# Optimization experiments

Hardware: AMD Instinct MI355X
Metric: run time of the kernel (lower is better)

## Reference

```python
import jax, jax.numpy as jnp
import numpy as np
import math

H = 16          # num_heads
MAX_REL = 512   # max_relative_positions


def setup_inputs() -> dict:
    key = jax.random.key(0)
    ks = jax.random.split(key, 8)
    B, N, Hd = 1, 2048, 1024
    s = 0.05  # keep activations numerically tame
    return {
        "hidden_states": jax.random.normal(ks[0], (B, N, Hd), jnp.float32),
        "attention_mask": jnp.ones((B, N, N), jnp.int32),
        "W_in": jax.random.normal(ks[1], (3 * Hd, Hd), jnp.float32) * s,
        "q_bias": jax.random.normal(ks[2], (Hd,), jnp.float32) * s,
        "v_bias": jax.random.normal(ks[3], (Hd,), jnp.float32) * s,
        "W_pos": jax.random.normal(ks[4], (Hd, Hd), jnp.float32) * s,
        "W_posq": jax.random.normal(ks[5], (Hd, Hd), jnp.float32) * s,
        "b_posq": jax.random.normal(ks[6], (Hd,), jnp.float32) * s,
        "rel_emb": jax.random.normal(ks[7], (2 * MAX_REL, Hd), jnp.float32) * s,
    }


def reference(hidden_states, attention_mask, W_in, q_bias, v_bias, W_pos, W_posq, b_posq, rel_emb):
    B, N, Hd = hidden_states.shape
    d = Hd // H
    span = min(N, MAX_REL)
    scale_factor = 3  # 1 + c2p + p2c

    # in_proj then DeBERTa-style head split: [B,N,H,3d] -> chunk last dim
    qp = jnp.einsum('bnk,ok->bno', hidden_states, W_in).reshape(B, N, H, 3 * d)
    q, k, v = jnp.split(qp, 3, axis=-1)            # each [B,N,H,d]
    q = q.transpose(0, 2, 1, 3)                    # [B,H,N,d]
    k = k.transpose(0, 2, 1, 3)
    v = v.transpose(0, 2, 1, 3)
    q = q + q_bias.reshape(H, d)[None, :, None, :]
    v = v + v_bias.reshape(H, d)[None, :, None, :]

    q = q / math.sqrt(d * scale_factor)
    scores = jnp.einsum('bhid,bhjd->bhij', q, k)   # content-to-content

    # relative position table, sliced around center
    rel = rel_emb[MAX_REL - span: MAX_REL + span]                     # [2span,Hd]
    pos_k = jnp.einsum('sk,ok->so', rel, W_pos).reshape(2 * span, H, d).transpose(1, 0, 2)   # [H,2span,d]
    pos_q = (jnp.einsum('sk,ok->so', rel, W_posq) + b_posq).reshape(2 * span, H, d).transpose(1, 0, 2)
    pos_q = pos_q / math.sqrt(d * scale_factor)

    rp = jnp.arange(N)[:, None] - jnp.arange(N)[None, :]              # [N,N] rel pos q->k
    c2p_idx = jnp.clip(rp + span, 0, 2 * span - 1)                    # [N,N]
    p2c_idx = jnp.clip(-rp + span, 0, 2 * span - 1)

    # content-to-position: gather along span axis
    c2p = jnp.einsum('bhid,hsd->bhis', q, pos_k)                      # [B,H,N,2span]
    c2p = jnp.take_along_axis(c2p, c2p_idx[None, None], axis=-1)      # [B,H,N,N]

    # position-to-content: gather then transpose(-1,-2)
    p2c = jnp.einsum('bhjd,hsd->bhjs', k, pos_q)                      # [B,H,N,2span]
    p2c = jnp.take_along_axis(p2c, p2c_idx[None, None], axis=-1)      # [B,H,j,i]
    p2c = p2c.transpose(0, 1, 3, 2)                                   # [B,H,i,j]

    scores = scores + c2p + p2c

    # XSoftmax: mask-fill with dtype min, softmax, re-zero masked
    mask = attention_mask.astype(bool)[:, None]                       # [B,1,N,N]
    neg = jnp.finfo(scores.dtype).min
    probs = jax.nn.softmax(jnp.where(mask, scores, neg), axis=-1)
    probs = jnp.where(mask, probs, 0.0)

    ctx = jnp.einsum('bhij,bhjd->bhid', probs, v)                     # [B,H,N,d]
    return ctx.transpose(0, 2, 1, 3).reshape(B, N, Hd)
```

## Files before the change

kernel.cpp:

```cpp
#include <hip/hip_runtime.h>

#define SEQ   2048
#define HID   1024
#define NHEAD 16
#define DH    64
#define S2    1024

typedef short bf16x8 __attribute__((ext_vector_type(8)));
typedef float f32x4  __attribute__((ext_vector_type(4)));

static __device__ __forceinline__ short f2bf(float f) {
    unsigned u = __float_as_uint(f);
    unsigned r = (u + 0x7fffu + ((u >> 16) & 1u)) >> 16;
    return (short)r;
}
static __device__ __forceinline__ float bf2f(short h) {
    return __uint_as_float(((unsigned)(unsigned short)h) << 16);
}
static __device__ __forceinline__ int wbase(int a) {
    int b = a < 0 ? 0 : (a > 952 ? 952 : a);
    return b & ~7;
}


__global__ __launch_bounds__(256) void cvt_bf16_k(const float* __restrict__ in,
                                                  short* __restrict__ out, int n8) {
    int idx = blockIdx.x * 256 + threadIdx.x;
    if (idx < n8) {
        const float4 a = ((const float4*)in)[idx * 2];
        const float4 b = ((const float4*)in)[idx * 2 + 1];
        bf16x8 r;
        r[0] = f2bf(a.x); r[1] = f2bf(a.y); r[2] = f2bf(a.z); r[3] = f2bf(a.w);
        r[4] = f2bf(b.x); r[5] = f2bf(b.y); r[6] = f2bf(b.z); r[7] = f2bf(b.w);
        ((bf16x8*)out)[idx] = r;
    }
}

__global__ __launch_bounds__(256) void cvt3_bf16_k(
    const float* __restrict__ in0, const float* __restrict__ in1, const float* __restrict__ in2,
    short* __restrict__ out0, short* __restrict__ out1, short* __restrict__ out2) {
    int b = blockIdx.x, sel = b >> 9;
    int idx = (b & 511) * 256 + threadIdx.x;
    const float* in = sel == 0 ? in0 : (sel == 1 ? in1 : in2);
    short* out = sel == 0 ? out0 : (sel == 1 ? out1 : out2);
    const float4 a = ((const float4*)in)[idx * 2];
    const float4 b4 = ((const float4*)in)[idx * 2 + 1];
    bf16x8 r;
    r[0] = f2bf(a.x); r[1] = f2bf(a.y); r[2] = f2bf(a.z); r[3] = f2bf(a.w);
    r[4] = f2bf(b4.x); r[5] = f2bf(b4.y); r[6] = f2bf(b4.z); r[7] = f2bf(b4.w);
    ((bf16x8*)out)[idx] = r;
}

__global__ __launch_bounds__(256) void maskflag_k(const int* __restrict__ amask, int* __restrict__ flags)
{
    __shared__ int sall[4], sany[4];
    const int jt = blockIdx.x, it = blockIdx.y;
    const int tid = threadIdx.x;
    const int r = tid >> 2, cseg = (tid & 3) << 4;
    const int4* rp = (const int4*)(amask + (size_t)(it * 64 + r) * SEQ + jt * 64 + cseg);
    int allnz = 1, anynz = 0;
    #pragma unroll
    for (int e = 0; e < 4; ++e) {
        int4 v = rp[e];
        allnz &= (v.x != 0) & (v.y != 0) & (v.z != 0) & (v.w != 0);
        anynz |= (v.x != 0) | (v.y != 0) | (v.z != 0) | (v.w != 0);
    }
    unsigned long long ba = __ballot(allnz != 0);
    unsigned long long bo = __ballot(anynz != 0);
    const int w = tid >> 6;
    if ((tid & 63) == 0) { sall[w] = (ba == ~0ull); sany[w] = (bo != 0ull); }
    __syncthreads();
    if (tid == 0) {
        int all4 = sall[0] & sall[1] & sall[2] & sall[3];
        int any4 = sany[0] | sany[1] | sany[2] | sany[3];
        flags[it * 32 + jt] = all4 ? 2 : (any4 ? 1 : 0);
    }
}

static __device__ __forceinline__ void gemm_tile(
    const short* __restrict__ Ag, int lda,
    const short* __restrict__ Bg, int ldb,
    int K, short* As, short* Bs, f32x4 (&acc)[4][2])
{
    const int tid = threadIdx.x;
    const int lane = tid & 63, w = tid >> 6;
    const int g = lane >> 4, ln = lane & 15;
    const int wm = (w >> 1) * 64, wn = (w & 1) * 32;
    for (int kt = 0; kt < K; kt += 64) {
        __syncthreads();
        #pragma unroll
        for (int it = 0; it < 4; ++it) {
            int c = it * 256 + tid;
            int r = c >> 3, cb = c & 7;
            uint4 v = *(const uint4*)(Ag + (size_t)r * lda + kt + ((cb ^ (r & 7)) << 3));
            *(uint4*)(As + r * 64 + cb * 8) = v;
        }
        #pragma unroll
        for (int it = 0; it < 2; ++it) {
            int c = it * 256 + tid;
            int r = c >> 3, cb = c & 7;
            uint4 v = *(const uint4*)(Bg + (size_t)r * ldb + kt + ((cb ^ (r & 7)) << 3));
            *(uint4*)(Bs + r * 64 + cb * 8) = v;
        }
        __syncthreads();
        #pragma unroll
        for (int k0 = 0; k0 < 2; ++k0) {
            bf16x8 bfr[2];
            #pragma unroll
            for (int nf = 0; nf < 2; ++nf) {
                int rr = wn + nf * 16 + ln;
                int kc = (k0 * 4 + g) ^ (rr & 7);
                bfr[nf] = *(const bf16x8*)(Bs + rr * 64 + kc * 8);
            }
            #pragma unroll
            for (int mf = 0; mf < 4; ++mf) {
                int rr = wm + mf * 16 + ln;
                int kc = (k0 * 4 + g) ^ (rr & 7);
                bf16x8 afr = *(const bf16x8*)(As + rr * 64 + kc * 8);
                #pragma unroll
                for (int nf = 0; nf < 2; ++nf)
                    acc[mf][nf] = __builtin_amdgcn_mfma_f32_16x16x32_bf16(afr, bfr[nf], acc[mf][nf], 0, 0, 0);
            }
        }
    }
}

__global__ __launch_bounds__(256) void qkv_mfma_k(
    const short* __restrict__ hid, const short* __restrict__ win,
    const float* __restrict__ q_bias, const float* __restrict__ v_bias,
    short* __restrict__ qT, short* __restrict__ kT, short* __restrict__ vTt)
{
    __shared__ __align__(16) short As[128 * 64];
    __shared__ __align__(16) short Bs[64 * 64];
    const int tid = threadIdx.x, lane = tid & 63, w = tid >> 6;
    const int g = lane >> 4, ln = lane & 15;
    const int wm = (w >> 1) * 64, wn = (w & 1) * 32;
    const int m0 = blockIdx.y * 128, n0 = blockIdx.x * 64;
    f32x4 acc[4][2] = {};
    gemm_tile(hid + (size_t)m0 * HID, HID, win + (size_t)n0 * HID, HID, HID, As, Bs, acc);
    const float inv_s = 0.07216878364870323f * 1.4426950408889634f;
    #pragma unroll
    for (int nf = 0; nf < 2; ++nf) {
        const int n = n0 + wn + nf * 16 + ln;
        const int h = n / 192, c = n % 192;
        #pragma unroll
        for (int mf = 0; mf < 4; ++mf) {
            const int mb = m0 + wm + mf * 16 + 4 * g;
            if (c < 64) {
                float qb = q_bias[h * 64 + c];
                #pragma unroll
                for (int reg = 0; reg < 4; ++reg)
                    qT[((size_t)h * SEQ + mb + reg) * DH + c] = f2bf((acc[mf][nf][reg] + qb) * inv_s);
            } else if (c < 128) {
                #pragma unroll
                for (int reg = 0; reg < 4; ++reg)
                    kT[((size_t)h * SEQ + mb + reg) * DH + (c - 64)] = f2bf(acc[mf][nf][reg]);
            } else {
                float vb = v_bias[h * 64 + (c - 128)];
                short4 s4;
                s4.x = f2bf(acc[mf][nf][0] + vb);
                s4.y = f2bf(acc[mf][nf][1] + vb);
                s4.z = f2bf(acc[mf][nf][2] + vb);
                s4.w = f2bf(acc[mf][nf][3] + vb);
                *(short4*)(vTt + ((size_t)h * DH + (c - 128)) * SEQ + mb) = s4;
            }
        }
    }
}

__global__ __launch_bounds__(256) void pos_mfma_k(
    const short* __restrict__ rel, const short* __restrict__ wpos, const short* __restrict__ wposq,
    const float* __restrict__ b_posq, short* __restrict__ posk, short* __restrict__ posq)
{
    __shared__ __align__(16) short As[128 * 64];
    __shared__ __align__(16) short Bs[64 * 64];
    const int tid = threadIdx.x, lane = tid & 63, w = tid >> 6;
    const int g = lane >> 4, ln = lane & 15;
    const int wm = (w >> 1) * 64, wn = (w & 1) * 32;
    const int m0 = blockIdx.y * 128, n0 = blockIdx.x * 64;
    const int which = blockIdx.z;
    const short* Bg = (which ? wposq : wpos) + (size_t)n0 * HID;
    f32x4 acc[4][2] = {};
    gemm_tile(rel + (size_t)m0 * HID, HID, Bg, HID, HID, As, Bs, acc);
    const float inv_s = 0.07216878364870323f * 1.4426950408889634f;
    #pragma unroll
    for (int mf = 0; mf < 4; ++mf) {
        #pragma unroll
        for (int nf = 0; nf < 2; ++nf) {
            #pragma unroll
            for (int reg = 0; reg < 4; ++reg) {
                int s = m0 + wm + mf * 16 + 4 * g + reg;
                int o = n0 + wn + nf * 16 + ln;
                int h = o >> 6, c = o & 63;
                float v = acc[mf][nf][reg];
                if (which) posq[((size_t)h * S2 + s) * DH + c] = f2bf((v + b_posq[o]) * inv_s);
                else       posk[((size_t)h * S2 + s) * DH + c] = f2bf(v);
            }
        }
    }
}

__global__ __launch_bounds__(256) void band_mfma_k(
    const short* __restrict__ qT, const short* __restrict__ kT,
    const short* __restrict__ posk, const short* __restrict__ posq,
    short* __restrict__ c2p, short* __restrict__ p2c)
{
    __shared__ __align__(16) short Xs[128 * 64];
    __shared__ __align__(16) short Ps[64 * 64];
    const int tid = threadIdx.x, lane = tid & 63, w = tid >> 6;
    const int g = lane >> 4, ln = lane & 15;
    const int m0 = blockIdx.y * 128, n0 = blockIdx.x * 64;
    const int head = blockIdx.z >> 1, which = blockIdx.z & 1;
    const short* Xg = (which ? kT : qT) + (size_t)head * SEQ * DH + (size_t)m0 * DH;
    const short* Pg = (which ? posq : posk) + (size_t)head * S2 * DH + (size_t)n0 * DH;
    short* outb = (which ? p2c : c2p) + (size_t)head * SEQ * S2;
    #pragma unroll
    for (int it = 0; it < 4; ++it) {
        int c = it * 256 + tid;
        int r = c >> 3, cb = c & 7;
        *(uint4*)(Xs + r * 64 + cb * 8) = *(const uint4*)(Xg + (size_t)r * DH + ((cb ^ (r & 7)) << 3));
    }
    #pragma unroll
    for (int it = 0; it < 2; ++it) {
        int c = it * 256 + tid;
        int r = c >> 3, cb = c & 7;
        *(uint4*)(Ps + r * 64 + cb * 8) = *(const uint4*)(Pg + (size_t)r * DH + ((cb ^ (r & 7)) << 3));
    }
    __syncthreads();
    const int wm = w * 32;
    f32x4 acc[2][4] = {};
    #pragma unroll
    for (int k0 = 0; k0 < 2; ++k0) {
        bf16x8 af[4];
        #pragma unroll
        for (int nf = 0; nf < 4; ++nf) {
            int rr = nf * 16 + ln;
            af[nf] = *(const bf16x8*)(Ps + rr * 64 + (((k0 * 4 + g) ^ (rr & 7)) << 3));
        }
        #pragma unroll
        for (int mf = 0; mf < 2; ++mf) {
            int rr = wm + mf * 16 + ln;
            bf16x8 xf = *(const bf16x8*)(Xs + rr * 64 + (((k0 * 4 + g) ^ (rr & 7)) << 3));
            #pragma unroll
            for (int nf = 0; nf < 4; ++nf)
                acc[mf][nf] = __builtin_amdgcn_mfma_f32_16x16x32_bf16(af[nf], xf, acc[mf][nf], 0, 0, 0);
        }
    }
    #pragma unroll
    for (int mf = 0; mf < 2; ++mf) {
        const int m = m0 + wm + mf * 16 + ln;
        #pragma unroll
        for (int nf = 0; nf < 4; ++nf) {
            short4 s4;
            s4.x = f2bf(acc[mf][nf][0]);
            s4.y = f2bf(acc[mf][nf][1]);
            s4.z = f2bf(acc[mf][nf][2]);
            s4.w = f2bf(acc[mf][nf][3]);
            *(short4*)(outb + (size_t)m * S2 + n0 + nf * 16 + 4 * g) = s4;
        }
    }
}

__global__ __launch_bounds__(256) void attn_mfma_k(
    const short* __restrict__ qT, const short* __restrict__ kT, const short* __restrict__ vTt,
    const short* __restrict__ c2p, const short* __restrict__ p2c,
    const int* __restrict__ amask, const int* __restrict__ flags,
    float* __restrict__ out)
{
    __shared__ __align__(16) char pool[69632];
    short* const lds = (short*)pool;
    const int tid = threadIdx.x, lane = tid & 63, w = tid >> 6;
    const int g = lane >> 4, ln = lane & 15;
    const int h = blockIdx.y, it = blockIdx.x;
    const int i0 = it * 64;
    const int iw = i0 + w * 16;
    const short* qh = qT + (size_t)h * SEQ * DH;
    const short* kh = kT + (size_t)h * SEQ * DH;
    const short* vh = vTt + (size_t)h * DH * SEQ;
    const short* ch = c2p + (size_t)h * SEQ * S2;
    const short* ph = p2c + (size_t)h * SEQ * S2;

    bf16x8 aq[2];
    aq[0] = *(const bf16x8*)(qh + (size_t)(iw + ln) * DH + 0  + g * 8);
    aq[1] = *(const bf16x8*)(qh + (size_t)(iw + ln) * DH + 32 + g * 8);

    f32x4 o4[4] = {};
    float mrow = -1.0e30f, lrow = 0.f;

    const int fbase = it * 32;
    const int r0 = tid >> 3,          cb0 = tid & 7;
    const int r1 = (256 + tid) >> 3,  cb1 = tid & 7;
    const int ksw0 = (cb0 ^ (r0 & 7)) << 3, ksw1 = (cb1 ^ (r1 & 7)) << 3;
    const int wr = tid >> 2, wu = (tid & 3) * 16;

    uint4 kr0, kr1, vr0, vr1, cw0, cw1, pw0, pw1, cw2, pw2;

    auto issue = [&](int jt) {
        const int j0 = jt * 64;
        kr0 = *(const uint4*)(kh + (size_t)(j0 + r0) * DH + ksw0);
        vr0 = *(const uint4*)(vh + (size_t)r0 * SEQ + j0 + ksw0);
        kr1 = *(const uint4*)(kh + (size_t)(j0 + r1) * DH + ksw1);
        vr1 = *(const uint4*)(vh + (size_t)r1 * SEQ + j0 + ksw1);
        int bc = wbase(i0 + wr - j0 + 449);
        cw0 = *(const uint4*)(ch + (size_t)(i0 + wr) * S2 + bc + wu);
        cw1 = *(const uint4*)(ch + (size_t)(i0 + wr) * S2 + bc + wu + 8);
        int bp = wbase(i0 - j0 - wr + 512);
        pw0 = *(const uint4*)(ph + (size_t)(j0 + wr) * S2 + bp + wu);
        pw1 = *(const uint4*)(ph + (size_t)(j0 + wr) * S2 + bp + wu + 8);
        if (tid < 64) {
            int bc2 = wbase(i0 + tid - j0 + 449);
            cw2 = *(const uint4*)(ch + (size_t)(i0 + tid) * S2 + bc2 + 64);
            int bp2 = wbase(i0 - j0 - tid + 512);
            pw2 = *(const uint4*)(ph + (size_t)(j0 + tid) * S2 + bp2 + 64);
        }
    };
    auto commit = [&](int bo) {
        short* Ks  = lds + bo;
        short* Vs  = lds + bo + 4096;
        short* Phw = lds + bo + 8192;
        short* Chw = lds + bo + 12800;
        *(uint4*)(Ks + r0 * 64 + cb0 * 8) = kr0;
        *(uint4*)(Vs + r0 * 64 + cb0 * 8) = vr0;
        *(uint4*)(Ks + r1 * 64 + cb1 * 8) = kr1;
        *(uint4*)(Vs + r1 * 64 + cb1 * 8) = vr1;
        *(uint4*)(Chw + wr * 72 + wu) = cw0;
        *(uint4*)(Chw + wr * 72 + wu + 8) = cw1;
        *(uint4*)(Phw + wr * 72 + wu) = pw0;
        *(uint4*)(Phw + wr * 72 + wu + 8) = pw1;
        if (tid < 64) {
            *(uint4*)(Chw + tid * 72 + 64) = cw2;
            *(uint4*)(Phw + tid * 72 + 64) = pw2;
        }
    };

    issue(0);
    int flag_cur = flags[fbase];
    commit(0);
    __syncthreads();

    const int il = w * 16 + ln;
    const int i  = i0 + il;

    int bo = 0;
    for (int t = 0; t < 32; ++t) {
        const int j0 = t * 64;
        int flag_next = 0;
        if (t < 31) { flag_next = flags[fbase + t + 1]; issue(t + 1); }

        short* Ks  = lds + bo;
        short* Vs  = lds + bo + 4096;
        short* Phw = lds + bo + 8192;
        short* Chw = lds + bo + 12800;
        short* Psw = Chw + w * 1152;

        if (flag_cur != 0) {
            f32x4 sfr[4];
            #pragma unroll
            for (int nf = 0; nf < 4; ++nf) sfr[nf] = (f32x4){0.f, 0.f, 0.f, 0.f};
            __builtin_amdgcn_s_setprio(1);
            #pragma unroll
            for (int k0 = 0; k0 < 2; ++k0) {
                #pragma unroll
                for (int nf = 0; nf < 4; ++nf) {
                    int rr = nf * 16 + ln;
                    bf16x8 ak = *(const bf16x8*)(Ks + rr * 64 + (((k0 * 4 + g) ^ (rr & 7)) << 3));
                    sfr[nf] = __builtin_amdgcn_mfma_f32_16x16x32_bf16(ak, aq[k0], sfr[nf], 0, 0, 0);
                }
            }
            __builtin_amdgcn_s_setprio(0);

            const int d = i0 - j0;
            float p[4][4];
            if (d >= -448 && d <= 384 && flag_cur == 2) {
                const int a = i - j0 + 449;
                const short* Cb = Chw + il * 72 + (a & 7) - 4 * g;
                const int cg = d + 512 - 4 * g;
                const int pbase = il + 288 * g;
                const int pb0 = pbase + (cg & 7);
                const int pb1 = pbase + ((cg - 1) & 7);
                const int pb2 = pbase + ((cg - 2) & 7);
                const int pb3 = pbase + ((cg - 3) & 7);
                #pragma unroll
                for (int nf = 0; nf < 4; ++nf) {
                    p[nf][0] = sfr[nf][0] + bf2f(Cb[63 - 16 * nf - 0]) + bf2f(Phw[pb0 + 1152 * nf + 0]);
                    p[nf][1] = sfr[nf][1] + bf2f(Cb[63 - 16 * nf - 1]) + bf2f(Phw[pb1 + 1152 * nf + 72]);
                    p[nf][2] = sfr[nf][2] + bf2f(Cb[63 - 16 * nf - 2]) + bf2f(Phw[pb2 + 1152 * nf + 144]);
                    p[nf][3] = sfr[nf][3] + bf2f(Cb[63 - 16 * nf - 3]) + bf2f(Phw[pb3 + 1152 * nf + 216]);
                }
            } else if (flag_cur == 2 && (d <= -576 || d >= 576)) {
                const int q = d < 0 ? 0 : 71;
                const float cb = bf2f(Chw[il * 72 + q]);
                #pragma unroll
                for (int nf = 0; nf < 4; ++nf) {
                    const int pb = (16 * nf + 4 * g) * 72 + q;
                    p[nf][0] = sfr[nf][0] + cb + bf2f(Phw[pb]);
                    p[nf][1] = sfr[nf][1] + cb + bf2f(Phw[pb + 72]);
                    p[nf][2] = sfr[nf][2] + cb + bf2f(Phw[pb + 144]);
                    p[nf][3] = sfr[nf][3] + cb + bf2f(Phw[pb + 216]);
                }
            } else {
                const short* Crow = Chw + il * 72 - wbase(i - j0 + 449);
                const int Cc = i0 - j0 + 512;
                #pragma unroll
                for (int nf = 0; nf < 4; ++nf) {
                    #pragma unroll
                    for (int reg = 0; reg < 4; ++reg) {
                        int jr = 16 * nf + 4 * g + reg;
                        int s = i - (j0 + jr) + 512; s = s < 0 ? 0 : (s > 1023 ? 1023 : s);
                        int wbp = Cc - jr; wbp = wbp < 0 ? 0 : (wbp > 952 ? 952 : wbp); wbp &= ~7;
                        float sc = sfr[nf][reg] + bf2f(Crow[s]) + bf2f(Phw[jr * 72 + (s - wbp)]);
                        if (flag_cur != 2)
                            sc = amask[(size_t)i * SEQ + (j0 + jr)] ? sc : -1.0e30f;
                        p[nf][reg] = sc;
                    }
                }
            }

            float mx = p[0][0];
            #pragma unroll
            for (int nf = 0; nf < 4; ++nf)
                #pragma unroll
                for (int reg = 0; reg < 4; ++reg) mx = fmaxf(mx, p[nf][reg]);
            mx = fmaxf(mx, __shfl_xor(mx, 16, 64));
            mx = fmaxf(mx, __shfl_xor(mx, 32, 64));
            float nm = fmaxf(mrow, mx);
            float sc, rs = 0.f;
            if (flag_cur == 2) {
                sc = exp2f(mrow - nm);
                #pragma unroll
                for (int nf = 0; nf < 4; ++nf)
                    #pragma unroll
                    for (int reg = 0; reg < 4; ++reg) {
                        float e = exp2f(p[nf][reg] - nm);
                        p[nf][reg] = e; rs += e;
                    }
            } else {
                bool live = nm > -5.0e29f;
                sc = live ? exp2f(mrow - nm) : 1.f;
                #pragma unroll
                for (int nf = 0; nf < 4; ++nf)
                    #pragma unroll
                    for (int reg = 0; reg < 4; ++reg) {
                        float e = live ? exp2f(p[nf][reg] - nm) : 0.f;
                        p[nf][reg] = e; rs += e;
                    }
            }
            rs += __shfl_xor(rs, 16, 64);
            rs += __shfl_xor(rs, 32, 64);
            lrow = lrow * sc + rs;
            mrow = nm;

            #pragma unroll
            for (int nf = 0; nf < 4; ++nf) {
                short4 s4;
                s4.x = f2bf(p[nf][0]); s4.y = f2bf(p[nf][1]);
                s4.z = f2bf(p[nf][2]); s4.w = f2bf(p[nf][3]);
                *(short4*)(Psw + ln * 72 + 16 * nf + 4 * g) = s4;
            }

            #pragma unroll
            for (int mf = 0; mf < 4; ++mf)
                #pragma unroll
                for (int reg = 0; reg < 4; ++reg) o4[mf][reg] *= sc;

            __builtin_amdgcn_s_setprio(1);
            #pragma unroll
            for (int k0 = 0; k0 < 2; ++k0) {
                bf16x8 bp = *(const bf16x8*)(Psw + ln * 72 + k0 * 32 + g * 8);
                #pragma unroll
                for (int mf = 0; mf < 4; ++mf) {
                    int rr = mf * 16 + ln;
                    bf16x8 av = *(const bf16x8*)(Vs + rr * 64 + (((k0 * 4 + g) ^ (rr & 7)) << 3));
                    o4[mf] = __builtin_amdgcn_mfma_f32_16x16x32_bf16(av, bp, o4[mf], 0, 0, 0);
                }
            }
            __builtin_amdgcn_s_setprio(0);
        }

        if (t < 31) commit(bo ^ 17408);
        __syncthreads();
        bo ^= 17408;
        flag_cur = flag_next;
    }

    float rinv = (mrow > -5.0e29f && lrow > 0.f) ? 1.f / lrow : 0.f;
    __syncthreads();
    float* Tf = (float*)pool;
    #pragma unroll
    for (int mf = 0; mf < 4; ++mf)
        #pragma unroll
        for (int reg = 0; reg < 4; ++reg)
            Tf[(w * 16 + ln) * 68 + mf * 16 + 4 * g + reg] = o4[mf][reg] * rinv;
    __syncthreads();
    {
        const int r = tid >> 2, sgm = (tid & 3) << 4;
        float* dst = out + (size_t)(i0 + r) * HID + h * 64 + sgm;
        #pragma unroll
        for (int k = 0; k < 4; ++k)
            ((float4*)dst)[k] = *(float4*)(Tf + r * 68 + sgm + k * 4);
    }
}

extern "C" void kernel_launch(void* const* d_in, const int* in_sizes, int n_in,
                              void* d_out, int out_size, void* d_ws, size_t ws_size,
                              hipStream_t stream)
{
    const float* hidden  = (const float*)d_in[0];
    const int*   amask   = (const int*)  d_in[1];
    const float* W_in    = (const float*)d_in[2];
    const float* q_bias  = (const float*)d_in[3];
    const float* v_bias  = (const float*)d_in[4];
    const float* W_pos   = (const float*)d_in[5];
    const float* W_posq  = (const float*)d_in[6];
    const float* b_posq  = (const float*)d_in[7];
    const float* rel_emb = (const float*)d_in[8];
    float* out = (float*)d_out;

    short* ws = (short*)d_ws;
    short* qT   = ws;
    short* kT   = ws + 2097152;
    short* vTt  = ws + 4194304;
    short* c2p  = ws + 6291456;
    short* p2c  = ws + 39845888;
    short* scr      = ws + 73400320;
    short* hid_bf   = scr;
    short* win_bf   = scr + 2097152;
    short* rel_bf   = scr;
    short* wpos_bf  = scr + 1048576;
    short* wposq_bf = scr + 2097152;
    short* posk     = scr + 3145728;
    short* posq     = scr + 4194304;
    int*   flags    = (int*)(scr + 8650752);

    cvt_bf16_k<<<1024, 256, 0, stream>>>(hidden, hid_bf, 262144);
    cvt_bf16_k<<<1536, 256, 0, stream>>>(W_in, win_bf, 393216);
    maskflag_k<<<dim3(32, 32), 256, 0, stream>>>(amask, flags);
    qkv_mfma_k<<<dim3(48, 16), 256, 0, stream>>>(hid_bf, win_bf, q_bias, v_bias, qT, kT, vTt);
    cvt3_bf16_k<<<1536, 256, 0, stream>>>(rel_emb, W_pos, W_posq, rel_bf, wpos_bf, wposq_bf);
    pos_mfma_k<<<dim3(16, 8, 2), 256, 0, stream>>>(rel_bf, wpos_bf, wposq_bf, b_posq, posk, posq);
    band_mfma_k<<<dim3(16, 16, 32), 256, 0, stream>>>(qT, kT, posk, posq, c2p, p2c);
    attn_mfma_k<<<dim3(32, 16), 256, 0, stream>>>(qT, kT, vTt, c2p, p2c, amask, flags, out);
}
```

Baseline: 190.6 us.

## Merge conversion, mask-flag and projection kernels; use packed bf16 convert instruction

Merges the three fp32-to-bf16 conversion kernels and the mask-flag kernel into one launch, and the QKV and positional projection GEMMs into one launch. The scratch buffers are moved apart so the two projections no longer alias each other. Several bf16 store paths now use the hardware v_cvt_pk_bf16_f32 packed conversion instead of manual rounding. The aim is to cut four launches and their tail effects and to shorten epilogue instruction counts, at the cost of more scratch memory.

```diff
diff --git a/kernel.cpp b/kernel.cpp
--- a/kernel.cpp
+++ b/kernel.cpp
@@ -17,63 +17,65 @@
 static __device__ __forceinline__ float bf2f(short h) {
     return __uint_as_float(((unsigned)(unsigned short)h) << 16);
 }
+static __device__ __forceinline__ unsigned cvtpk(float lo, float hi) {
+    unsigned r;
+    asm("v_cvt_pk_bf16_f32 %0, %1, %2" : "=v"(r) : "v"(lo), "v"(hi));
+    return r;
+}
 static __device__ __forceinline__ int wbase(int a) {
     int b = a < 0 ? 0 : (a > 952 ? 952 : a);
     return b & ~7;
 }
 
 
-__global__ __launch_bounds__(256) void cvt_bf16_k(const float* __restrict__ in,
-                                                  short* __restrict__ out, int n8) {
-    int idx = blockIdx.x * 256 + threadIdx.x;
-    if (idx < n8) {
+__global__ __launch_bounds__(256) void prep_k(
+    const float* __restrict__ hid_f, const float* __restrict__ win_f,
+    const float* __restrict__ rel_f, const float* __restrict__ wpos_f,
+    const float* __restrict__ wposq_f, const int* __restrict__ amask,
+    short* __restrict__ hid_bf, short* __restrict__ win_bf,
+    short* __restrict__ rel_bf, short* __restrict__ wpos_bf,
+    short* __restrict__ wposq_bf, int* __restrict__ flags)
+{
+    __shared__ int sall[4], sany[4];
+    const int b = blockIdx.x, tid = threadIdx.x;
+    if (b < 4096) {
+        const float* in; short* out; int idx;
+        if (b < 1024)      { in = hid_f;  out = hid_bf;  idx = b * 256 + tid; }
+        else if (b < 2560) { in = win_f;  out = win_bf;  idx = (b - 1024) * 256 + tid; }
+        else {
+            int t = b - 2560, sel = t >> 9;
+            in  = sel == 0 ? rel_f  : (sel == 1 ? wpos_f  : wposq_f);
+            out = sel == 0 ? rel_bf : (sel == 1 ? wpos_bf : wposq_bf);
+            idx = (t & 511) * 256 + tid;
+        }
         const float4 a = ((const float4*)in)[idx * 2];
-        const float4 b = ((const float4*)in)[idx * 2 + 1];
+        const float4 b4 = ((const float4*)in)[idx * 2 + 1];
         bf16x8 r;
         r[0] = f2bf(a.x); r[1] = f2bf(a.y); r[2] = f2bf(a.z); r[3] = f2bf(a.w);
-        r[4] = f2bf(b.x); r[5] = f2bf(b.y); r[6] = f2bf(b.z); r[7] = f2bf(b.w);
+        r[4] = f2bf(b4.x); r[5] = f2bf(b4.y); r[6] = f2bf(b4.z); r[7] = f2bf(b4.w);
         ((bf16x8*)out)[idx] = r;
-    }
-}
-
-__global__ __launch_bounds__(256) void cvt3_bf16_k(
-    const float* __restrict__ in0, const float* __restrict__ in1, const float* __restrict__ in2,
-    short* __restrict__ out0, short* __restrict__ out1, short* __restrict__ out2) {
-    int b = blockIdx.x, sel = b >> 9;
-    int idx = (b & 511) * 256 + threadIdx.x;
-    const float* in = sel == 0 ? in0 : (sel == 1 ? in1 : in2);
-    short* out = sel == 0 ? out0 : (sel == 1 ? out1 : out2);
-    const float4 a = ((const float4*)in)[idx * 2];
-    const float4 b4 = ((const float4*)in)[idx * 2 + 1];
-    bf16x8 r;
-    r[0] = f2bf(a.x); r[1] = f2bf(a.y); r[2] = f2bf(a.z); r[3] = f2bf(a.w);
-    r[4] = f2bf(b4.x); r[5] = f2bf(b4.y); r[6] = f2bf(b4.z); r[7] = f2bf(b4.w);
-    ((bf16x8*)out)[idx] = r;
-}
-
-__global__ __launch_bounds__(256) void maskflag_k(const int* __restrict__ amask, int* __restrict__ flags)
-{
-    __shared__ int sall[4], sany[4];
-    const int jt = blockIdx.x, it = blockIdx.y;
-    const int tid = threadIdx.x;
-    const int r = tid >> 2, cseg = (tid & 3) << 4;
-    const int4* rp = (const int4*)(amask + (size_t)(it * 64 + r) * SEQ + jt * 64 + cseg);
-    int allnz = 1, anynz = 0;
-    #pragma unroll
-    for (int e = 0; e < 4; ++e) {
-        int4 v = rp[e];
-        allnz &= (v.x != 0) & (v.y != 0) & (v.z != 0) & (v.w != 0);
-        anynz |= (v.x != 0) | (v.y != 0) | (v.z != 0) | (v.w != 0);
-    }
-    unsigned long long ba = __ballot(allnz != 0);
-    unsigned long long bo = __ballot(anynz != 0);
-    const int w = tid >> 6;
-    if ((tid & 63) == 0) { sall[w] = (ba == ~0ull); sany[w] = (bo != 0ull); }
-    __syncthreads();
-    if (tid == 0) {
-        int all4 = sall[0] & sall[1] & sall[2] & sall[3];
-        int any4 = sany[0] | sany[1] | sany[2] | sany[3];
-        flags[it * 32 + jt] = all4 ? 2 : (any4 ? 1 : 0);
+    } else {
+        const int mb = b - 4096;
+        const int jt = mb & 31, it = mb >> 5;
+        const int r = tid >> 2, cseg = (tid & 3) << 4;
+        const int4* rp = (const int4*)(amask + (size_t)(it * 64 + r) * SEQ + jt * 64 + cseg);
+        int allnz = 1, anynz = 0;
+        #pragma unroll
+        for (int e = 0; e < 4; ++e) {
+            int4 v = rp[e];
+            allnz &= (v.x != 0) & (v.y != 0) & (v.z != 0) & (v.w != 0);
+            anynz |= (v.x != 0) | (v.y != 0) | (v.z != 0) | (v.w != 0);
+        }
+        unsigned long long ba = __ballot(allnz != 0);
+        unsigned long long bo = __ballot(anynz != 0);
+        const int w = tid >> 6;
+        if ((tid & 63) == 0) { sall[w] = (ba == ~0ull); sany[w] = (bo != 0ull); }
+        __syncthreads();
+        if (tid == 0) {
+            int all4 = sall[0] & sall[1] & sall[2] & sall[3];
+            int any4 = sany[0] | sany[1] | sany[2] | sany[3];
+            flags[it * 32 + jt] = all4 ? 2 : (any4 ? 1 : 0);
+        }
     }
 }
 
@@ -125,76 +127,71 @@
     }
 }
 
-__global__ __launch_bounds__(256) void qkv_mfma_k(
+__global__ __launch_bounds__(256) void qkvpos_k(
     const short* __restrict__ hid, const short* __restrict__ win,
     const float* __restrict__ q_bias, const float* __restrict__ v_bias,
-    short* __restrict__ qT, short* __restrict__ kT, short* __restrict__ vTt)
+    const short* __restrict__ rel, const short* __restrict__ wpos, const short* __restrict__ wposq,
+    const float* __restrict__ b_posq,
+    short* __restrict__ qT, short* __restrict__ kT, short* __restrict__ vTt,
+    short* __restrict__ posk, short* __restrict__ posq)
 {
     __shared__ __align__(16) short As[128 * 64];
     __shared__ __align__(16) short Bs[64 * 64];
     const int tid = threadIdx.x, lane = tid & 63, w = tid >> 6;
     const int g = lane >> 4, ln = lane & 15;
     const int wm = (w >> 1) * 64, wn = (w & 1) * 32;
-    const int m0 = blockIdx.y * 128, n0 = blockIdx.x * 64;
+    const int x = blockIdx.x;
+    const float inv_s = 0.07216878364870323f * 1.4426950408889634f;
     f32x4 acc[4][2] = {};
-    gemm_tile(hid + (size_t)m0 * HID, HID, win + (size_t)n0 * HID, HID, HID, As, Bs, acc);
-    const float inv_s = 0.07216878364870323f * 1.4426950408889634f;
-    #pragma unroll
-    for (int nf = 0; nf < 2; ++nf) {
-        const int n = n0 + wn + nf * 16 + ln;
-        const int h = n / 192, c = n % 192;
+
+    if (x < 768) {
+        const int bx = x % 48, by = x / 48;
+        const int m0 = by * 128, n0 = bx * 64;
+        gemm_tile(hid + (size_t)m0 * HID, HID, win + (size_t)n0 * HID, HID, HID, As, Bs, acc);
+        #pragma unroll
+        for (int nf = 0; nf < 2; ++nf) {
+            const int n = n0 + wn + nf * 16 + ln;
+            const int h = n / 192, c = n % 192;
+            #pragma unroll
+            for (int mf = 0; mf < 4; ++mf) {
+                const int mb = m0 + wm + mf * 16 + 4 * g;
+                if (c < 64) {
+                    float qb = q_bias[h * 64 + c];
+                    #pragma unroll
+                    for (int reg = 0; reg < 4; ++reg)
+                        qT[((size_t)h * SEQ + mb + reg) * DH + c] = f2bf((acc[mf][nf][reg] + qb) * inv_s);
+                } else if (c < 128) {
+                    #pragma unroll
+                    for (int reg = 0; reg < 4; ++reg)
+                        kT[((size_t)h * SEQ + mb + reg) * DH + (c - 64)] = f2bf(acc[mf][nf][reg]);
+                } else {
+                    float vb = v_bias[h * 64 + (c - 128)];
+                    uint2 u;
+                    u.x = cvtpk(acc[mf][nf][0] + vb, acc[mf][nf][1] + vb);
+                    u.y = cvtpk(acc[mf][nf][2] + vb, acc[mf][nf][3] + vb);
+                    *(uint2*)(vTt + ((size_t)h * DH + (c - 128)) * SEQ + mb) = u;
+                }
+            }
+        }
+    } else {
+        const int t = x - 768;
+        const int which = t >> 7, rest = t & 127;
+        const int m0 = (rest / 16) * 128, n0 = (rest % 16) * 64;
+        const short* Bg = (which ? wposq : wpos) + (size_t)n0 * HID;
+        gemm_tile(rel + (size_t)m0 * HID, HID, Bg, HID, HID, As, Bs, acc);
         #pragma unroll
         for (int mf = 0; mf < 4; ++mf) {
-            const int mb = m0 + wm + mf * 16 + 4 * g;
-            if (c < 64) {
-                float qb = q_bias[h * 64 + c];
-                #pragma unroll
-                for (int reg = 0; reg < 4; ++reg)
-                    qT[((size_t)h * SEQ + mb + reg) * DH + c] = f2bf((acc[mf][nf][reg] + qb) * inv_s);
-            } else if (c < 128) {
-                #pragma unroll
-                for (int reg = 0; reg < 4; ++reg)
-                    kT[((size_t)h * SEQ + mb + reg) * DH + (c - 64)] = f2bf(acc[mf][nf][reg]);
-            } else {
-                float vb = v_bias[h * 64 + (c - 128)];
-                short4 s4;
-                s4.x = f2bf(acc[mf][nf][0] + vb);
-                s4.y = f2bf(acc[mf][nf][1] + vb);
-                s4.z = f2bf(acc[mf][nf][2] + vb);
-                s4.w = f2bf(acc[mf][nf][3] + vb);
-                *(short4*)(vTt + ((size_t)h * DH + (c - 128)) * SEQ + mb) = s4;
-            }
-        }
-    }
-}
-
-__global__ __launch_bounds__(256) void pos_mfma_k(
-    const short* __restrict__ rel, const short* __restrict__ wpos, const short* __restrict__ wposq,
-    const float* __restrict__ b_posq, short* __restrict__ posk, short* __restrict__ posq)
-{
-    __shared__ __align__(16) short As[128 * 64];
-    __shared__ __align__(16) short Bs[64 * 64];
-    const int tid = threadIdx.x, lane = tid & 63, w = tid >> 6;
-    const int g = lane >> 4, ln = lane & 15;
-    const int wm = (w >> 1) * 64, wn = (w & 1) * 32;
-    const int m0 = blockIdx.y * 128, n0 = blockIdx.x * 64;
-    const int which = blockIdx.z;
-    const short* Bg = (which ? wposq : wpos) + (size_t)n0 * HID;
-    f32x4 acc[4][2] = {};
-    gemm_tile(rel + (size_t)m0 * HID, HID, Bg, HID, HID, As, Bs, acc);
-    const float inv_s = 0.07216878364870323f * 1.4426950408889634f;
-    #pragma unroll
-    for (int mf = 0; mf < 4; ++mf) {
-        #pragma unroll
-        for (int nf = 0; nf < 2; ++nf) {
-            #pragma unroll
-            for (int reg = 0; reg < 4; ++reg) {
-                int s = m0 + wm + mf * 16 + 4 * g + reg;
-                int o = n0 + wn + nf * 16 + ln;
-                int h = o >> 6, c = o & 63;
-                float v = acc[mf][nf][reg];
-                if (which) posq[((size_t)h * S2 + s) * DH + c] = f2bf((v + b_posq[o]) * inv_s);
-                else       posk[((size_t)h * S2 + s) * DH + c] = f2bf(v);
+            #pragma unroll
+            for (int nf = 0; nf < 2; ++nf) {
+                #pragma unroll
+                for (int reg = 0; reg < 4; ++reg) {
+                    int s = m0 + wm + mf * 16 + 4 * g + reg;
+                    int o = n0 + wn + nf * 16 + ln;
+                    int h = o >> 6, c = o & 63;
+                    float v = acc[mf][nf][reg];
+                    if (which) posq[((size_t)h * S2 + s) * DH + c] = f2bf((v + b_posq[o]) * inv_s);
+                    else       posk[((size_t)h * S2 + s) * DH + c] = f2bf(v);
+                }
             }
         }
     }
@@ -251,12 +248,10 @@
         const int m = m0 + wm + mf * 16 + ln;
         #pragma unroll
         for (int nf = 0; nf < 4; ++nf) {
-            short4 s4;
-            s4.x = f2bf(acc[mf][nf][0]);
-            s4.y = f2bf(acc[mf][nf][1]);
-            s4.z = f2bf(acc[mf][nf][2]);
-            s4.w = f2bf(acc[mf][nf][3]);
-            *(short4*)(outb + (size_t)m * S2 + n0 + nf * 16 + 4 * g) = s4;
+            uint2 u;
+            u.x = cvtpk(acc[mf][nf][0], acc[mf][nf][1]);
+            u.y = cvtpk(acc[mf][nf][2], acc[mf][nf][3]);
+            *(uint2*)(outb + (size_t)m * S2 + n0 + nf * 16 + 4 * g) = u;
         }
     }
 }
@@ -452,10 +447,10 @@
 
             #pragma unroll
             for (int nf = 0; nf < 4; ++nf) {
-                short4 s4;
-                s4.x = f2bf(p[nf][0]); s4.y = f2bf(p[nf][1]);
-                s4.z = f2bf(p[nf][2]); s4.w = f2bf(p[nf][3]);
-                *(short4*)(Psw + ln * 72 + 16 * nf + 4 * g) = s4;
+                uint2 u;
+                u.x = cvtpk(p[nf][0], p[nf][1]);
+                u.y = cvtpk(p[nf][2], p[nf][3]);
+                *(uint2*)(Psw + ln * 72 + 16 * nf + 4 * g) = u;
             }
 
             #pragma unroll
@@ -525,19 +520,18 @@
     short* scr      = ws + 73400320;
     short* hid_bf   = scr;
     short* win_bf   = scr + 2097152;
-    short* rel_bf   = scr;
-    short* wpos_bf  = scr + 1048576;
-    short* wposq_bf = scr + 2097152;
-    short* posk     = scr + 3145728;
-    short* posq     = scr + 4194304;
-    int*   flags    = (int*)(scr + 8650752);
-
-    cvt_bf16_k<<<1024, 256, 0, stream>>>(hidden, hid_bf, 262144);
-    cvt_bf16_k<<<1536, 256, 0, stream>>>(W_in, win_bf, 393216);
-    maskflag_k<<<dim3(32, 32), 256, 0, stream>>>(amask, flags);
-    qkv_mfma_k<<<dim3(48, 16), 256, 0, stream>>>(hid_bf, win_bf, q_bias, v_bias, qT, kT, vTt);
-    cvt3_bf16_k<<<1536, 256, 0, stream>>>(rel_emb, W_pos, W_posq, rel_bf, wpos_bf, wposq_bf);
-    pos_mfma_k<<<dim3(16, 8, 2), 256, 0, stream>>>(rel_bf, wpos_bf, wposq_bf, b_posq, posk, posq);
+    short* rel_bf   = scr + 5242880;
+    short* wpos_bf  = scr + 6291456;
+    short* wposq_bf = scr + 7340032;
+    short* posk     = scr + 8388608;
+    short* posq     = scr + 9437184;
+    int*   flags    = (int*)(scr + 10485760);
+
+    prep_k<<<5120, 256, 0, stream>>>(hidden, W_in, rel_emb, W_pos, W_posq, amask,
+                                     hid_bf, win_bf, rel_bf, wpos_bf, wposq_bf, flags);
+    qkvpos_k<<<1024, 256, 0, stream>>>(hid_bf, win_bf, q_bias, v_bias,
+                                       rel_bf, wpos_bf, wposq_bf, b_posq,
+                                       qT, kT, vTt, posk, posq);
     band_mfma_k<<<dim3(16, 16, 32), 256, 0, stream>>>(qT, kT, posk, posq, c2p, p2c);
     attn_mfma_k<<<dim3(32, 16), 256, 0, stream>>>(qT, kT, vTt, c2p, p2c, amask, flags, out);
 }
```

Result: faster. 174.2 us (-8.6%).
